# Optimization experiments

Measured on AMD Instinct MI355X. Metric: run time of the kernel, lower is better.

Reference implementation:

```python
import jax, jax.numpy as jnp
from jax import lax
import numpy as np
import math

MAXV = 127.0  # 2**(8-1)-1, signed int8 narrow range

def setup_inputs() -> dict:
    key = jax.random.key(0)
    kx, kw, kb = jax.random.split(key, 3)
    B, Cin, H, W = 32, 128, 56, 56
    Cout, K = 256, 3
    x = jax.random.normal(kx, (B, Cin, H, W), dtype=jnp.float32)
    # kaiming_uniform_(a=sqrt(5)) -> bound = sqrt(6 / ((1+5) * fan_in)) = 1/sqrt(fan_in)
    fan_in = Cin * K * K
    bound = 1.0 / math.sqrt(fan_in)
    weight = jax.random.uniform(kw, (Cout, Cin, K, K), dtype=jnp.float32,
                                minval=-bound, maxval=bound)
    bias = jax.random.uniform(kb, (Cout,), dtype=jnp.float32,
                              minval=-bound, maxval=bound)
    return {"x": x, "weight": weight, "bias": bias}

def _quantize_i8(t):
    """Max-calibrated signed 8-bit quantization (fake_quant=False -> integer output)."""
    amax = jnp.max(jnp.abs(t))
    scale = MAXV / amax
    q = jnp.clip(jnp.round(t * scale), -MAXV, MAXV).astype(jnp.int8)
    return q, scale

def reference(x, weight, bias):
    # quantize activations and weights to int8
    qx, sx = _quantize_i8(x)
    qw, sw = _quantize_i8(weight)
    # exact int8 conv with int32 accumulation (systolic exact path), stride=1, pad=1
    out_i32 = lax.conv_general_dilated(
        qx, qw,
        window_strides=(1, 1),
        padding=((1, 1), (1, 1)),
        dimension_numbers=("NCHW", "OIHW", "NCHW"),
        preferred_element_type=jnp.int32,
    )
    # dequantize and add bias
    out = out_i32.astype(jnp.float32) / (sx * sw)
    return out + bias[None, :, None, None]
```

## Files before the change

kernel.cpp:

```cpp
#include <hip/hip_runtime.h>


#define B_    32
#define CIN   128
#define H_    56
#define W_    56
#define COUT  256
#define HP    58
#define WP    58
#define HWP   (H_*W_)
#define NPIX  (B_*HWP)
#define NCHUNK 18
#define ACHUNK 16384

typedef int int4v __attribute__((ext_vector_type(4)));

__device__ __forceinline__ void gld_lds16(const void* g, void* l) {
    __builtin_amdgcn_global_load_lds(
        (const __attribute__((address_space(1))) unsigned int*)g,
        (__attribute__((address_space(3))) unsigned int*)l, 16, 0, 0);
}

__global__ __launch_bounds__(256) void amax_kernel(const float4* __restrict__ x, long n4x,
                                                   const float4* __restrict__ wt, long n4w,
                                                   unsigned* __restrict__ scales) {
    const float4* p; long n4; unsigned* slot; long start, stride;
    if (blockIdx.x < 2048) {
        p = x; n4 = n4x; slot = scales;
        start = (long)blockIdx.x * 256 + threadIdx.x; stride = 2048L * 256;
    } else {
        p = wt; n4 = n4w; slot = scales + 1;
        start = (long)(blockIdx.x - 2048) * 256 + threadIdx.x; stride = 128L * 256;
    }
    float m = 0.f;
    for (long i = start; i < n4; i += stride) {
        float4 v = p[i];
        m = fmaxf(m, fmaxf(fmaxf(fabsf(v.x), fabsf(v.y)), fmaxf(fabsf(v.z), fabsf(v.w))));
    }
    __shared__ float red[256];
    red[threadIdx.x] = m; __syncthreads();
    for (int s = 128; s > 0; s >>= 1) {
        if (threadIdx.x < s) red[threadIdx.x] = fmaxf(red[threadIdx.x], red[threadIdx.x + s]);
        __syncthreads();
    }
    if (threadIdx.x == 0) atomicMax(slot, __float_as_uint(red[0]));
}

__global__ __launch_bounds__(256) void quant_x_kernel(const float* __restrict__ x,
        const unsigned* __restrict__ scales, signed char* __restrict__ xq) {
    const int bh = blockIdx.x;
    const int b = bh / H_, h = bh % H_;
    const float sx = 127.0f / __uint_as_float(scales[0]);
    __shared__ int ldsq[W_ * 33];
    const int tid = threadIdx.x;

    int4 z; z.x = 0; z.y = 0; z.z = 0; z.w = 0;
    int4* prow = (int4*)(xq + ((long)b * HP + h + 1) * WP * CIN);
    if (tid < 8) prow[tid] = z;
    else if (tid < 16) prow[456 + tid - 8] = z;
    if (h == 0) {
        int4* r0 = (int4*)(xq + (long)b * HP * WP * CIN);
        for (int i = tid; i < 464; i += 256) r0[i] = z;
    } else if (h == H_ - 1) {
        int4* rt = (int4*)(xq + ((long)b * HP + 57) * WP * CIN);
        for (int i = tid; i < 464; i += 256) rt[i] = z;
    }

    const int w = tid & 63;
    const int chi = tid >> 6;
    if (w < W_) {
        const float* xb = x + (long)b * CIN * HWP + h * W_ + w;
#pragma unroll
        for (int it = 0; it < 8; ++it) {
            const int c4 = it * 4 + chi;
            int pk = 0;
#pragma unroll
            for (int u = 0; u < 4; ++u) {
                float v = xb[(long)(c4 * 4 + u) * HWP];
                float q = fminf(127.f, fmaxf(-127.f, rintf(v * sx)));
                pk |= ((int)q & 0xff) << (u * 8);
            }
            ldsq[w * 33 + c4] = pk;
        }
    }
    __syncthreads();
    int4* dst = (int4*)(xq + (((long)b * HP + h + 1) * WP + 1) * CIN);
    for (int idx = tid; idx < W_ * 8; idx += 256) {
        const int ww = idx >> 3, c16 = idx & 7;
        int4 v;
        v.x = ldsq[ww * 33 + c16 * 4 + 0];
        v.y = ldsq[ww * 33 + c16 * 4 + 1];
        v.z = ldsq[ww * 33 + c16 * 4 + 2];
        v.w = ldsq[ww * 33 + c16 * 4 + 3];
        dst[ww * 8 + c16] = v;
    }
}

__global__ __launch_bounds__(256) void quant_w_kernel(const float* __restrict__ wt,
        const unsigned* __restrict__ scales, signed char* __restrict__ wq) {
    const int id = blockIdx.x * 256 + threadIdx.x;
    if (id >= COUT * 9 * 32) return;
    const float sw = 127.0f / __uint_as_float(scales[1]);
    const int co = id / 288;
    const int r  = id % 288;
    const int t  = r / 32;
    const int c4 = r % 32;
    int pk = 0;
#pragma unroll
    for (int u = 0; u < 4; ++u) {
        float v = wt[(co * CIN + c4 * 4 + u) * 9 + t];
        float q = fminf(127.f, fmaxf(-127.f, rintf(v * sw)));
        pk |= ((int)q & 0xff) << (u * 8);
    }
    const int k = t * CIN + c4 * 4;
    const int chunk = k >> 6;
    const int off = k & 63;
    *(int*)(wq + (long)chunk * ACHUNK + (off >> 4) * 4096 + co * 16 + (off & 15)) = pk;
}

__global__ __launch_bounds__(512, 4) void conv_kernel(
        const signed char* __restrict__ xq, const signed char* __restrict__ wq,
        const float* __restrict__ bias, const unsigned* __restrict__ scales,
        float* __restrict__ out) {
    __shared__ signed char As[3][16384];
    __shared__ signed char Bs[3][8192];

    const int tid = threadIdx.x;
    const int lane = tid & 63;
    const int wv = tid >> 6;
    const int ln = lane & 15;
    const int g  = lane >> 4;

    const int wco = wv >> 1;
    const int wpx = wv & 1;

    const int bid = blockIdx.x;
    const int wg  = (bid & 7) * 98 + (bid >> 3);
    const int px_blk = wg * 128;

    const int aoff0 = wv * 2048 + lane * 16;
    const int aoff1 = aoff0 + 1024;

    const int gB = wv >> 1, halfB = wv & 1;
    const int pxs = px_blk + halfB * 64 + lane;
    const int bS = pxs / HWP, hwS = pxs % HWP;
    const int hS = hwS / W_, wS = hwS % W_;
    const signed char* srcB = xq + ((bS * HP + hS) * WP + wS) * CIN + gB * 16;
    const int ldsB = gB * 2048 + halfB * 1024 + lane * 16;

#define STAGE(c) { \
    const int tap_ = (c) >> 1; \
    const int toff_ = ((tap_ / 3) * WP + (tap_ % 3)) * CIN + ((c) & 1) * 64; \
    const int bf_ = (c) % 3; \
    gld_lds16(wq + (c) * ACHUNK + aoff0, &As[bf_][aoff0]); \
    gld_lds16(wq + (c) * ACHUNK + aoff1, &As[bf_][aoff1]); \
    gld_lds16(srcB + toff_, &Bs[bf_][ldsB]); }

#define LDA_(i) (*(const int4v*)&As[buf][g * 4096 + (wco * 64 + (i) * 16 + ln) * 16])
#define LDB_(j) (*(const int4v*)&Bs[buf][g * 2048 + (wpx * 64 + (j) * 16 + ln) * 16])
#define MM(i, j, A, Bv) acc[i][j] = __builtin_amdgcn_mfma_i32_16x16x64_i8(A, Bv, acc[i][j], 0, 0, 0)

#define CHUNK(c, VM) { \
    const int buf = (c) % 3; \
    asm volatile("s_waitcnt vmcnt(" #VM ")\n\ts_barrier" ::: "memory"); \
    __builtin_amdgcn_sched_barrier(0); \
    if ((c) + 2 < NCHUNK) STAGE((c) + 2); \
    int4v Bf0 = LDB_(0), Bf1 = LDB_(1), Bf2 = LDB_(2), Bf3 = LDB_(3); \
    int4v Af0 = LDA_(0), Af1 = LDA_(1); \
    __builtin_amdgcn_s_setprio(1); \
    MM(0, 0, Af0, Bf0); MM(0, 1, Af0, Bf1); MM(0, 2, Af0, Bf2); MM(0, 3, Af0, Bf3); \
    MM(1, 0, Af1, Bf0); MM(1, 1, Af1, Bf1); MM(1, 2, Af1, Bf2); MM(1, 3, Af1, Bf3); \
    __builtin_amdgcn_s_setprio(0); \
    asm volatile("s_barrier" ::: "memory"); \
    __builtin_amdgcn_sched_barrier(0); \
    int4v Af2 = LDA_(2), Af3 = LDA_(3); \
    __builtin_amdgcn_s_setprio(1); \
    MM(2, 0, Af2, Bf0); MM(2, 1, Af2, Bf1); MM(2, 2, Af2, Bf2); MM(2, 3, Af2, Bf3); \
    MM(3, 0, Af3, Bf0); MM(3, 1, Af3, Bf1); MM(3, 2, Af3, Bf2); MM(3, 3, Af3, Bf3); \
    __builtin_amdgcn_s_setprio(0); }

    int4v acc[4][4] = {};
    STAGE(0);
    STAGE(1);
    CHUNK(0, 3)  CHUNK(1, 3)  CHUNK(2, 3)  CHUNK(3, 3)  CHUNK(4, 3)  CHUNK(5, 3)
    CHUNK(6, 3)  CHUNK(7, 3)  CHUNK(8, 3)  CHUNK(9, 3)  CHUNK(10, 3) CHUNK(11, 3)
    CHUNK(12, 3) CHUNK(13, 3) CHUNK(14, 3) CHUNK(15, 3) CHUNK(16, 3) CHUNK(17, 0)
#undef CHUNK
#undef MM
#undef LDA_
#undef LDB_
#undef STAGE

    const float ax = __uint_as_float(scales[0]);
    const float aw = __uint_as_float(scales[1]);
    const float inv = 1.0f / ((127.0f / ax) * (127.0f / aw));

#pragma unroll
    for (int i = 0; i < 4; ++i) {
        const int co = wco * 64 + i * 16 + g * 4;
#pragma unroll
        for (int r = 0; r < 4; ++r) {
            const float bsv = bias[co + r];
#pragma unroll
            for (int j = 0; j < 4; ++j) {
                const int px = px_blk + wpx * 64 + j * 16 + ln;
                const int b = px / HWP, hw = px % HWP;
                out[((long)(b * COUT + co + r)) * HWP + hw] = (float)acc[i][j][r] * inv + bsv;
            }
        }
    }
}

extern "C" void kernel_launch(void* const* d_in, const int* in_sizes, int n_in,
                              void* d_out, int out_size, void* d_ws, size_t ws_size,
                              hipStream_t stream) {
    const float* x  = (const float*)d_in[0];
    const float* wt = (const float*)d_in[1];
    const float* bs = (const float*)d_in[2];
    float* out = (float*)d_out;

    unsigned* scales = (unsigned*)d_ws;
    const size_t XQ_OFF   = 256;
    const size_t XQ_BYTES = (size_t)B_ * HP * WP * CIN;
    signed char* xq = (signed char*)d_ws + XQ_OFF;
    signed char* wq = xq + XQ_BYTES;

    hipMemsetAsync(d_ws, 0, 8, stream);

    const long n4x = (long)B_ * CIN * H_ * W_ / 4;
    const long n4w = (long)COUT * CIN * 9 / 4;
    amax_kernel<<<2176, 256, 0, stream>>>((const float4*)x, n4x, (const float4*)wt, n4w, scales);

    quant_x_kernel<<<B_ * H_, 256, 0, stream>>>(x, scales, xq);
    quant_w_kernel<<<(COUT * 9 * 32 + 255) / 256, 256, 0, stream>>>(wt, scales, wq);

    conv_kernel<<<NPIX / 128, 512, 0, stream>>>(xq, wq, bs, scales, out);
}
```

Before: 214.6 us.

## Stage conv epilogue through LDS for float4 stores and drop mid-chunk barrier

The output epilogue now writes the int32 accumulators, already scaled, into a padded LDS tile. It then reads them back so that each thread emits coalesced float4 stores along the pixel dimension, with bias added at store time. The shared-memory buffers are merged into one array so the epilogue can reuse the A/B staging space. In the main loop, all four A fragments are loaded up front and the extra mid-chunk s_barrier and sched_barriers are removed, cutting synchronisation. The cost is extra LDS traffic and barriers in the epilogue, higher register pressure from holding more fragments, and a possibly misaligned 16-byte LDS read caused by the 130-float row stride.

```diff
diff --git a/kernel.cpp b/kernel.cpp
--- a/kernel.cpp
+++ b/kernel.cpp
@@ -122,8 +122,7 @@
         const signed char* __restrict__ xq, const signed char* __restrict__ wq,
         const float* __restrict__ bias, const unsigned* __restrict__ scales,
         float* __restrict__ out) {
-    __shared__ signed char As[3][16384];
-    __shared__ signed char Bs[3][8192];
+    __shared__ signed char smem[73728];
 
     const int tid = threadIdx.x;
     const int lane = tid & 63;
@@ -152,29 +151,23 @@
     const int tap_ = (c) >> 1; \
     const int toff_ = ((tap_ / 3) * WP + (tap_ % 3)) * CIN + ((c) & 1) * 64; \
     const int bf_ = (c) % 3; \
-    gld_lds16(wq + (c) * ACHUNK + aoff0, &As[bf_][aoff0]); \
-    gld_lds16(wq + (c) * ACHUNK + aoff1, &As[bf_][aoff1]); \
-    gld_lds16(srcB + toff_, &Bs[bf_][ldsB]); }
-
-#define LDA_(i) (*(const int4v*)&As[buf][g * 4096 + (wco * 64 + (i) * 16 + ln) * 16])
-#define LDB_(j) (*(const int4v*)&Bs[buf][g * 2048 + (wpx * 64 + (j) * 16 + ln) * 16])
+    gld_lds16(wq + (c) * ACHUNK + aoff0, &smem[bf_ * 16384 + aoff0]); \
+    gld_lds16(wq + (c) * ACHUNK + aoff1, &smem[bf_ * 16384 + aoff1]); \
+    gld_lds16(srcB + toff_, &smem[49152 + bf_ * 8192 + ldsB]); }
+
+#define LDA_(i) (*(const int4v*)&smem[buf * 16384 + g * 4096 + (wco * 64 + (i) * 16 + ln) * 16])
+#define LDB_(j) (*(const int4v*)&smem[49152 + buf * 8192 + g * 2048 + (wpx * 64 + (j) * 16 + ln) * 16])
 #define MM(i, j, A, Bv) acc[i][j] = __builtin_amdgcn_mfma_i32_16x16x64_i8(A, Bv, acc[i][j], 0, 0, 0)
 
 #define CHUNK(c, VM) { \
     const int buf = (c) % 3; \
     asm volatile("s_waitcnt vmcnt(" #VM ")\n\ts_barrier" ::: "memory"); \
-    __builtin_amdgcn_sched_barrier(0); \
     if ((c) + 2 < NCHUNK) STAGE((c) + 2); \
     int4v Bf0 = LDB_(0), Bf1 = LDB_(1), Bf2 = LDB_(2), Bf3 = LDB_(3); \
-    int4v Af0 = LDA_(0), Af1 = LDA_(1); \
+    int4v Af0 = LDA_(0), Af1 = LDA_(1), Af2 = LDA_(2), Af3 = LDA_(3); \
     __builtin_amdgcn_s_setprio(1); \
     MM(0, 0, Af0, Bf0); MM(0, 1, Af0, Bf1); MM(0, 2, Af0, Bf2); MM(0, 3, Af0, Bf3); \
     MM(1, 0, Af1, Bf0); MM(1, 1, Af1, Bf1); MM(1, 2, Af1, Bf2); MM(1, 3, Af1, Bf3); \
-    __builtin_amdgcn_s_setprio(0); \
-    asm volatile("s_barrier" ::: "memory"); \
-    __builtin_amdgcn_sched_barrier(0); \
-    int4v Af2 = LDA_(2), Af3 = LDA_(3); \
-    __builtin_amdgcn_s_setprio(1); \
     MM(2, 0, Af2, Bf0); MM(2, 1, Af2, Bf1); MM(2, 2, Af2, Bf2); MM(2, 3, Af2, Bf3); \
     MM(3, 0, Af3, Bf0); MM(3, 1, Af3, Bf1); MM(3, 2, Af3, Bf2); MM(3, 3, Af3, Bf3); \
     __builtin_amdgcn_s_setprio(0); }
@@ -195,19 +188,40 @@
     const float aw = __uint_as_float(scales[1]);
     const float inv = 1.0f / ((127.0f / ax) * (127.0f / aw));
 
-#pragma unroll
-    for (int i = 0; i < 4; ++i) {
-        const int co = wco * 64 + i * 16 + g * 4;
-#pragma unroll
-        for (int r = 0; r < 4; ++r) {
-            const float bsv = bias[co + r];
-#pragma unroll
-            for (int j = 0; j < 4; ++j) {
-                const int px = px_blk + wpx * 64 + j * 16 + ln;
-                const int b = px / HWP, hw = px % HWP;
-                out[((long)(b * COUT + co + r)) * HWP + hw] = (float)acc[i][j][r] * inv + bsv;
-            }
+    __syncthreads();
+    float* ldsT = (float*)smem;
+
+    const int c4 = tid & 31;
+    const int rsel = tid >> 5;
+    const int px4 = px_blk + c4 * 4;
+    const int bb = px4 / HWP, hw = px4 - bb * HWP;
+    float4* outb = (float4*)(out + (long)bb * COUT * HWP + hw);
+
+#pragma unroll
+    for (int p = 0; p < 2; ++p) {
+        if ((wv >> 2) == p) {
+            const int cl0 = (wco & 1) * 64;
+#pragma unroll
+            for (int i = 0; i < 4; ++i)
+#pragma unroll
+                for (int r = 0; r < 4; ++r) {
+                    const int cl = cl0 + i * 16 + g * 4 + r;
+#pragma unroll
+                    for (int j = 0; j < 4; ++j)
+                        ldsT[cl * 130 + wpx * 64 + j * 16 + ln] = (float)acc[i][j][r] * inv;
+                }
         }
+        __syncthreads();
+#pragma unroll
+        for (int it = 0; it < 8; ++it) {
+            const int row = it * 16 + rsel;
+            const int co = p * 128 + row;
+            float4 v = *(float4*)&ldsT[row * 130 + c4 * 4];
+            const float bsv = bias[co];
+            v.x += bsv; v.y += bsv; v.z += bsv; v.w += bsv;
+            outb[(long)co * (HWP / 4)] = v;
+        }
+        if (p == 0) __syncthreads();
     }
 }
 
```

New measurement: 214.5 us. About the same (-0.0%).
